# Performance work log

Hardware: AMD Instinct MI355X
Metric: run time of the kernel (lower is better)

Reference implementation:

```python
import jax, jax.numpy as jnp
import numpy as np
import math

C = 768; H = 12; B = 2; TX = 2048; TC = 2048

def setup_inputs() -> dict:
    key = jax.random.key(0)
    ks = jax.random.split(key, 20)
    w = lambda k, s: jax.random.normal(k, s, dtype=jnp.float32) * 0.02
    inp = {
        "x": jax.random.normal(ks[0], (B, TX, C), dtype=jnp.float32),
        "context": jax.random.normal(ks[1], (B, TC, C), dtype=jnp.float32),
        "ln1_g": jnp.ones((C,), jnp.float32), "ln1_b": jnp.zeros((C,), jnp.float32),
        "ln2_g": jnp.ones((C,), jnp.float32), "ln2_b": jnp.zeros((C,), jnp.float32),
        "ln3_g": jnp.ones((C,), jnp.float32), "ln3_b": jnp.zeros((C,), jnp.float32),
        "sa_wq": w(ks[2], (C, C)), "sa_bq": jnp.zeros((C,), jnp.float32),
        "sa_wk": w(ks[3], (C, C)), "sa_bk": jnp.zeros((C,), jnp.float32),
        "sa_wv": w(ks[4], (C, C)), "sa_bv": jnp.zeros((C,), jnp.float32),
        "sa_wo": w(ks[5], (C, C)), "sa_bo": jnp.zeros((C,), jnp.float32),
        "xa_wq": w(ks[6], (C, C)), "xa_bq": jnp.zeros((C,), jnp.float32),
        "xa_wk": w(ks[7], (C, C)), "xa_bk": jnp.zeros((C,), jnp.float32),
        "xa_wv": w(ks[8], (C, C)), "xa_bv": jnp.zeros((C,), jnp.float32),
        "xa_wo": w(ks[9], (C, C)), "xa_bo": jnp.zeros((C,), jnp.float32),
        "mlp_w1": w(ks[10], (C, 4 * C)), "mlp_b1": jnp.zeros((4 * C,), jnp.float32),
        "mlp_w2": w(ks[11], (4 * C, C)), "mlp_b2": jnp.zeros((C,), jnp.float32),
        "n_head": H,
    }
    return inp

def _layernorm(x, g, b, eps=1e-5):
    mu = jnp.mean(x, axis=-1, keepdims=True)
    var = jnp.mean(jnp.square(x - mu), axis=-1, keepdims=True)
    return (x - mu) * jax.lax.rsqrt(var + eps) * g + b

def _attn(xq, xkv, wq, bq, wk, bk, wv, bv, wo, bo, n_head):
    Bq, Tq, Cm = xq.shape
    Tk = xkv.shape[1]
    dh = Cm // n_head
    q = (xq @ wq + bq).reshape(Bq, Tq, n_head, dh)
    k = (xkv @ wk + bk).reshape(Bq, Tk, n_head, dh)
    v = (xkv @ wv + bv).reshape(Bq, Tk, n_head, dh)
    att = jnp.einsum('bqhd,bkhd->bhqk', q, k) * (1.0 / math.sqrt(dh))
    att = jax.nn.softmax(att, axis=-1)
    y = jnp.einsum('bhqk,bkhd->bqhd', att, v).reshape(Bq, Tq, Cm)
    return y @ wo + bo

def reference(x, context, ln1_g, ln1_b, ln2_g, ln2_b, ln3_g, ln3_b,
              sa_wq, sa_bq, sa_wk, sa_bk, sa_wv, sa_bv, sa_wo, sa_bo,
              xa_wq, xa_bq, xa_wk, xa_bk, xa_wv, xa_bv, xa_wo, xa_bo,
              mlp_w1, mlp_b1, mlp_w2, mlp_b2, n_head):
    # pre-LN residual self-attention
    x = x + _attn(_layernorm(x, ln1_g, ln1_b), _layernorm(x, ln1_g, ln1_b),
                  sa_wq, sa_bq, sa_wk, sa_bk, sa_wv, sa_bv, sa_wo, sa_bo, n_head)
    # pre-LN residual cross-attention (context not normalized, matching source)
    x = x + _attn(_layernorm(x, ln2_g, ln2_b), context,
                  xa_wq, xa_bq, xa_wk, xa_bk, xa_wv, xa_bv, xa_wo, xa_bo, n_head)
    # pre-LN residual MLP with exact (erf) GELU, as torch.nn.GELU default
    h = _layernorm(x, ln3_g, ln3_b)
    x = x + (jax.nn.gelu(h @ mlp_w1 + mlp_b1, approximate=False) @ mlp_w2 + mlp_b2)
    return (x, context)
```

## Files before the change

kernel.cpp:

```cpp
#include <hip/hip_runtime.h>
#include <hip/hip_bf16.h>
#include <math.h>

#define CDIM 768
#define HDIM 3072
#define NROWS 4096
#define TSEQ 2048
#define NHEAD 12

typedef unsigned short u16;
typedef unsigned int   u32;
typedef __attribute__((ext_vector_type(8))) short short8;
typedef __attribute__((ext_vector_type(4))) float f32x4;

#define QSCALE 0.18033688011112042f

static __device__ __forceinline__ u16 f2bf(float f) {
    u32 x = __float_as_uint(f);
    x += 0x7fffu + ((x >> 16) & 1u);
    return (u16)(x >> 16);
}
static __device__ __forceinline__ u32 cvt_pk_bf16(float lo, float hi) {
    u32 r;
    asm("v_cvt_pk_bf16_f32 %0, %1, %2" : "=v"(r) : "v"(lo), "v"(hi));
    return r;
}

#define GLL16(g, l)                                                            \
    __builtin_amdgcn_global_load_lds(                                          \
        (const __attribute__((address_space(1))) void*)(g),                    \
        (__attribute__((address_space(3))) void*)(l), 16, 0, 0)

__launch_bounds__(256)
__global__ void wtrans(const float* __restrict__ w, u16* __restrict__ wt,
                       int K, int N) {
    __shared__ float t[32][33];
    const int n0 = blockIdx.x * 32, k0 = blockIdx.y * 32;
    const int tx = threadIdx.x & 31, ty = threadIdx.x >> 5;
#pragma unroll
    for (int i = ty; i < 32; i += 8)
        t[i][tx] = w[(size_t)(k0 + i) * N + n0 + tx];
    __syncthreads();
#pragma unroll
    for (int i = ty; i < 32; i += 8)
        wt[(size_t)(n0 + i) * K + k0 + tx] = f2bf(t[tx][i]);
}

__launch_bounds__(256)
__global__ void cvt_copy(const float* __restrict__ in, u16* __restrict__ out,
                         int n4) {
    int i = blockIdx.x * 256 + threadIdx.x;
    if (i >= n4) return;
    float4 v = ((const float4*)in)[i];
    ushort4 o;
    o.x = f2bf(v.x); o.y = f2bf(v.y); o.z = f2bf(v.z); o.w = f2bf(v.w);
    ((ushort4*)out)[i] = o;
}

__launch_bounds__(256)
__global__ void ln_kernel(const float* __restrict__ x, const float* __restrict__ g,
                          const float* __restrict__ bta, u16* __restrict__ out) {
    const int row = blockIdx.x, tid = threadIdx.x;
    const float* xr = x + (size_t)row * CDIM;
    float v0 = xr[tid], v1 = xr[tid + 256], v2 = xr[tid + 512];
    __shared__ float red[8];
    float s = v0 + v1 + v2;
#pragma unroll
    for (int m = 1; m < 64; m <<= 1) s += __shfl_xor(s, m);
    if ((tid & 63) == 0) red[tid >> 6] = s;
    __syncthreads();
    const float mu = (red[0] + red[1] + red[2] + red[3]) * (1.f / CDIM);
    const float d0 = v0 - mu, d1 = v1 - mu, d2 = v2 - mu;
    float q = d0 * d0 + d1 * d1 + d2 * d2;
#pragma unroll
    for (int m = 1; m < 64; m <<= 1) q += __shfl_xor(q, m);
    if ((tid & 63) == 0) red[4 + (tid >> 6)] = q;
    __syncthreads();
    const float var = (red[4] + red[5] + red[6] + red[7]) * (1.f / CDIM);
    const float rstd = rsqrtf(var + 1e-5f);
    u16* orow = out + (size_t)row * CDIM;
    orow[tid]       = f2bf(d0 * rstd * g[tid]       + bta[tid]);
    orow[tid + 256] = f2bf(d1 * rstd * g[tid + 256] + bta[tid + 256]);
    orow[tid + 512] = f2bf(d2 * rstd * g[tid + 512] + bta[tid + 512]);
}

struct GemmArgs {
    const u16* A[3];
    const u16* BT[3];
    const float* bias[3];
    const float* res[3];
    void* out[3];
    float alpha[3];
    int M, N, K;
};

template <int EPI, int BM>
__launch_bounds__(256)
__global__ void gemm_bt(GemmArgs ga) {
    constexpr int MF = BM / 32;
    __shared__ u16 Abuf[BM * 32];
    __shared__ u16 Bbuf[128 * 32];
    const int z = blockIdx.z;
    const u16* __restrict__ A  = ga.A[z];
    const u16* __restrict__ BT = ga.BT[z];
    const float* __restrict__ bias = ga.bias[z];
    const float* __restrict__ res  = ga.res[z];
    void* outv = ga.out[z];
    const float alpha = ga.alpha[z];
    const int N = ga.N, K = ga.K;

    const int tid = threadIdx.x;
    const int lane = tid & 63, w = tid >> 6;
    const int m0 = blockIdx.x * BM, n0 = blockIdx.y * 128;
    const int wr = (w >> 1) * (BM / 2), wc = (w & 1) * 64;
    const int lr = lane & 15, lc = lane >> 4;

    const int srowA = w * (BM / 4) + (lane >> 2);
    const int srowB = w * 32 + (lane >> 2);
    const int scol = (lane & 3) * 8;
    const u16* Ag = A + (size_t)(m0 + srowA) * K + scol;
    const u16* Bg = BT + (size_t)(n0 + srowB) * K + scol;
    char* Ab = (char*)Abuf + w * (BM * 16);
    char* Bb = (char*)Bbuf + w * 2048;

    f32x4 acc[MF][4];
#pragma unroll
    for (int m = 0; m < MF; ++m)
#pragma unroll
        for (int n = 0; n < 4; ++n) acc[m][n] = (f32x4){0.f, 0.f, 0.f, 0.f};

    const int nk = K >> 5;
    for (int kt = 0; kt < nk; ++kt) {
        const int ko = kt * 32;
        GLL16(Ag + ko, Ab);
        if constexpr (BM == 128) GLL16(Ag + 16 * K + ko, Ab + 1024);
        GLL16(Bg + ko,          Bb);
        GLL16(Bg + 16 * K + ko, Bb + 1024);
        __syncthreads();
        short8 af[MF], bfv[4];
#pragma unroll
        for (int m = 0; m < MF; ++m)
            af[m] = *(const short8*)((const char*)Abuf +
                                     (size_t)(wr + m * 16 + lr) * 64 + lc * 16);
#pragma unroll
        for (int n = 0; n < 4; ++n)
            bfv[n] = *(const short8*)((const char*)Bbuf +
                                      (size_t)(wc + n * 16 + lr) * 64 + lc * 16);
#pragma unroll
        for (int m = 0; m < MF; ++m)
#pragma unroll
            for (int n = 0; n < 4; ++n)
                acc[m][n] = __builtin_amdgcn_mfma_f32_16x16x32_bf16(
                    af[m], bfv[n], acc[m][n], 0, 0, 0);
        __syncthreads();
    }

#pragma unroll
    for (int n = 0; n < 4; ++n) {
        const int gc = n0 + wc + n * 16 + lr;
        const float bs = bias[gc];
#pragma unroll
        for (int m = 0; m < MF; ++m) {
            const int gr = m0 + wr + m * 16 + lc * 4;
#pragma unroll
            for (int r = 0; r < 4; ++r) {
                float v = (acc[m][n][r] + bs) * alpha;
                const size_t idx = (size_t)(gr + r) * N + gc;
                if constexpr (EPI == 0) {
                    ((u16*)outv)[idx] = f2bf(v);
                } else if constexpr (EPI == 1) {
                    ((float*)outv)[idx] = res[idx] + v;
                } else {
                    float gel = 0.5f * v * (1.0f + erff(v * 0.70710678118654752f));
                    ((u16*)outv)[idx] = f2bf(gel);
                }
            }
        }
    }
}

__launch_bounds__(256)
__global__ void attn_kernel(const u16* __restrict__ Qb, const u16* __restrict__ Kb,
                            const u16* __restrict__ Vb, u16* __restrict__ Ob) {
    __shared__ u16 Klds[64 * 72];
    __shared__ u16 Vt[64 * 72];
    const int tid = threadIdx.x;
    const int lane = tid & 63, w = tid >> 6;
    const int lr = lane & 15, lc = lane >> 4;
    const int b = blockIdx.y / NHEAD, h = blockIdx.y % NHEAD;
    const size_t qrow0 = (size_t)b * TSEQ + blockIdx.x * 64 + w * 16;
    const size_t krow0 = (size_t)b * TSEQ;
    const int hc = h * 64;

    short8 qf0, qf1;
    {
        const u16* qp = Qb + (qrow0 + lr) * CDIM + hc + lc * 8;
        qf0 = *(const short8*)qp;
        qf1 = *(const short8*)(qp + 32);
    }
    f32x4 oacc[4];
#pragma unroll
    for (int r = 0; r < 4; ++r) oacc[r] = (f32x4){0.f, 0.f, 0.f, 0.f};
    float mrow = -3e38f, lrow = 0.f;

    const int stg_r = tid >> 2, stg_s = tid & 3;
    const u16* kg = Kb + (krow0 + stg_r) * CDIM + hc + stg_s * 16;
    const u16* vg = Vb + (krow0 + stg_r) * CDIM + hc + stg_s * 16;
    uint4 ka0 = *(const uint4*)kg, ka1 = *(const uint4*)(kg + 8);
    uint4 va0 = *(const uint4*)vg, va1 = *(const uint4*)(vg + 8);
    const int sig = ((stg_r >> 5) << 5) + (((stg_r >> 2) & 3) << 3) +
                    (((stg_r >> 4) & 1) << 2) + (stg_r & 3);
    char* vdst = (char*)Vt + ((2 * sig) ^ (stg_s << 5)) +
                 (size_t)(stg_s * 16) * 144;

    for (int kt = 0; kt < TSEQ / 64; ++kt) {
        __syncthreads();
        {
            *(uint4*)&Klds[stg_r * 72 + stg_s * 16]     = ka0;
            *(uint4*)&Klds[stg_r * 72 + stg_s * 16 + 8] = ka1;
            u16 tmp[16];
            *(uint4*)(tmp)     = va0;
            *(uint4*)(tmp + 8) = va1;
#pragma unroll
            for (int j = 0; j < 16; ++j)
                *(u16*)(vdst + (size_t)j * 144) = tmp[j];
        }
        if (kt < TSEQ / 64 - 1) {
            kg += 64 * CDIM; vg += 64 * CDIM;
            ka0 = *(const uint4*)kg; ka1 = *(const uint4*)(kg + 8);
            va0 = *(const uint4*)vg; va1 = *(const uint4*)(vg + 8);
        }
        __syncthreads();

        f32x4 sf[4];
#pragma unroll
        for (int fn = 0; fn < 4; ++fn) {
            const u16* kr = &Klds[(lr + fn * 16) * 72 + lc * 8];
            short8 kb0 = *(const short8*)kr;
            short8 kb1 = *(const short8*)(kr + 32);
            f32x4 t = (f32x4){0.f, 0.f, 0.f, 0.f};
            t = __builtin_amdgcn_mfma_f32_16x16x32_bf16(kb0, qf0, t, 0, 0, 0);
            t = __builtin_amdgcn_mfma_f32_16x16x32_bf16(kb1, qf1, t, 0, 0, 0);
            sf[fn] = t;
        }

        float pm;
        {
            float a0 = fmaxf(fmaxf(sf[0][0], sf[0][1]), fmaxf(sf[0][2], sf[0][3]));
            float a1 = fmaxf(fmaxf(sf[1][0], sf[1][1]), fmaxf(sf[1][2], sf[1][3]));
            float a2 = fmaxf(fmaxf(sf[2][0], sf[2][1]), fmaxf(sf[2][2], sf[2][3]));
            float a3 = fmaxf(fmaxf(sf[3][0], sf[3][1]), fmaxf(sf[3][2], sf[3][3]));
            pm = fmaxf(fmaxf(a0, a1), fmaxf(a2, a3));
            pm = fmaxf(pm, __shfl_xor(pm, 16));
            pm = fmaxf(pm, __shfl_xor(pm, 32));
        }
        const float mn = fmaxf(mrow, pm);
        const float corr = exp2f(mrow - mn);
        mrow = mn;
        float rs;
        {
#pragma unroll
            for (int fn = 0; fn < 4; ++fn)
#pragma unroll
                for (int r = 0; r < 4; ++r) sf[fn][r] = exp2f(sf[fn][r] - mn);
            float s0 = (sf[0][0] + sf[0][1]) + (sf[0][2] + sf[0][3]);
            float s1 = (sf[1][0] + sf[1][1]) + (sf[1][2] + sf[1][3]);
            float s2 = (sf[2][0] + sf[2][1]) + (sf[2][2] + sf[2][3]);
            float s3 = (sf[3][0] + sf[3][1]) + (sf[3][2] + sf[3][3]);
            rs = (s0 + s1) + (s2 + s3);
            rs += __shfl_xor(rs, 16);
            rs += __shfl_xor(rs, 32);
        }
        lrow = lrow * corr + rs;
#pragma unroll
        for (int fd = 0; fd < 4; ++fd)
#pragma unroll
            for (int r = 0; r < 4; ++r) oacc[fd][r] *= corr;

        int4 pw0, pw1;
        pw0.x = cvt_pk_bf16(sf[0][0], sf[0][1]);
        pw0.y = cvt_pk_bf16(sf[0][2], sf[0][3]);
        pw0.z = cvt_pk_bf16(sf[1][0], sf[1][1]);
        pw0.w = cvt_pk_bf16(sf[1][2], sf[1][3]);
        pw1.x = cvt_pk_bf16(sf[2][0], sf[2][1]);
        pw1.y = cvt_pk_bf16(sf[2][2], sf[2][3]);
        pw1.z = cvt_pk_bf16(sf[3][0], sf[3][1]);
        pw1.w = cvt_pk_bf16(sf[3][2], sf[3][3]);
        short8 pb0 = *(short8*)&pw0;
        short8 pb1 = *(short8*)&pw1;

#pragma unroll
        for (int fd = 0; fd < 4; ++fd) {
            const char* vtb = (const char*)Vt + (size_t)(lr + fd * 16) * 144;
            short8 vb0 = *(const short8*)(vtb + ((lc * 16) ^ (fd * 32)));
            short8 vb1 = *(const short8*)(vtb + ((lc * 16 + 64) ^ (fd * 32)));
            oacc[fd] = __builtin_amdgcn_mfma_f32_16x16x32_bf16(vb0, pb0, oacc[fd], 0, 0, 0);
            oacc[fd] = __builtin_amdgcn_mfma_f32_16x16x32_bf16(vb1, pb1, oacc[fd], 0, 0, 0);
        }
    }

    const float rl = 1.f / lrow;
    u16* obase = Ob + (qrow0 + lr) * CDIM + hc + lc * 4;
#pragma unroll
    for (int fd = 0; fd < 4; ++fd) {
        ushort4 o;
        o.x = f2bf(oacc[fd][0] * rl);
        o.y = f2bf(oacc[fd][1] * rl);
        o.z = f2bf(oacc[fd][2] * rl);
        o.w = f2bf(oacc[fd][3] * rl);
        *(ushort4*)(obase + fd * 16) = o;
    }
}

extern "C" void kernel_launch(void* const* d_in, const int* in_sizes, int n_in,
                              void* d_out, int out_size, void* d_ws, size_t ws_size,
                              hipStream_t stream) {
    const float* x     = (const float*)d_in[0];
    const float* ctx   = (const float*)d_in[1];
    const float* ln1g  = (const float*)d_in[2];
    const float* ln1b  = (const float*)d_in[3];
    const float* ln2g  = (const float*)d_in[4];
    const float* ln2b  = (const float*)d_in[5];
    const float* ln3g  = (const float*)d_in[6];
    const float* ln3b  = (const float*)d_in[7];
    const float* sa_wq = (const float*)d_in[8];
    const float* sa_bq = (const float*)d_in[9];
    const float* sa_wk = (const float*)d_in[10];
    const float* sa_bk = (const float*)d_in[11];
    const float* sa_wv = (const float*)d_in[12];
    const float* sa_bv = (const float*)d_in[13];
    const float* sa_wo = (const float*)d_in[14];
    const float* sa_bo = (const float*)d_in[15];
    const float* xa_wq = (const float*)d_in[16];
    const float* xa_bq = (const float*)d_in[17];
    const float* xa_wk = (const float*)d_in[18];
    const float* xa_bk = (const float*)d_in[19];
    const float* xa_wv = (const float*)d_in[20];
    const float* xa_bv = (const float*)d_in[21];
    const float* xa_wo = (const float*)d_in[22];
    const float* xa_bo = (const float*)d_in[23];
    const float* m_w1  = (const float*)d_in[24];
    const float* m_b1  = (const float*)d_in[25];
    const float* m_w2  = (const float*)d_in[26];
    const float* m_b2  = (const float*)d_in[27];

    float* out_x   = (float*)d_out;
    float* out_ctx = out_x + (size_t)NROWS * CDIM;

    const size_t SZ_ACT  = (size_t)NROWS * CDIM * 2;
    const size_t SZ_WBIG = (size_t)HDIM * CDIM * 2;
    const size_t SZ_R    = (size_t)NROWS * CDIM * 4;
    const size_t NEEDED  = 5 * SZ_ACT + SZ_R + SZ_WBIG;
    if (ws_size < NEEDED) return;

    char* ws = (char*)d_ws;
    u16* qb    = (u16*)(ws);
    u16* kb    = (u16*)(ws + 1 * SZ_ACT);
    u16* vb    = (u16*)(ws + 2 * SZ_ACT);
    u16* ctxb  = (u16*)(ws + 3 * SZ_ACT);
    u16* hb    = qb;
    u16* lnbuf = (u16*)(ws + 4 * SZ_ACT);
    u16* attB  = lnbuf;
    float* R   = (float*)(ws + 5 * SZ_ACT);
    u16* Wq    = (u16*)(ws + 5 * SZ_ACT + SZ_R);
    u16* Wk    = Wq + (size_t)CDIM * CDIM;
    u16* Wv    = Wk + (size_t)CDIM * CDIM;

    const dim3 tb(256);
    GemmArgs ga;

    hipMemcpyAsync(out_ctx, ctx, (size_t)NROWS * CDIM * 4,
                   hipMemcpyDeviceToDevice, stream);
    cvt_copy<<<dim3(3072), tb, 0, stream>>>(ctx, ctxb, NROWS * CDIM / 4);

    ln_kernel<<<dim3(NROWS), tb, 0, stream>>>(x, ln1g, ln1b, lnbuf);
    wtrans<<<dim3(24, 24), tb, 0, stream>>>(sa_wq, Wq, 768, 768);
    wtrans<<<dim3(24, 24), tb, 0, stream>>>(sa_wk, Wk, 768, 768);
    wtrans<<<dim3(24, 24), tb, 0, stream>>>(sa_wv, Wv, 768, 768);
    ga = GemmArgs{};
    ga.A[0] = lnbuf; ga.BT[0] = Wq; ga.bias[0] = sa_bq; ga.out[0] = qb; ga.alpha[0] = QSCALE;
    ga.A[1] = lnbuf; ga.BT[1] = Wk; ga.bias[1] = sa_bk; ga.out[1] = kb; ga.alpha[1] = 1.f;
    ga.A[2] = lnbuf; ga.BT[2] = Wv; ga.bias[2] = sa_bv; ga.out[2] = vb; ga.alpha[2] = 1.f;
    ga.M = 4096; ga.N = 768; ga.K = 768;
    gemm_bt<0, 128><<<dim3(32, 6, 3), tb, 0, stream>>>(ga);
    attn_kernel<<<dim3(32, 24), tb, 0, stream>>>(qb, kb, vb, attB);
    wtrans<<<dim3(24, 24), tb, 0, stream>>>(sa_wo, Wq, 768, 768);
    ga = GemmArgs{};
    ga.A[0] = attB; ga.BT[0] = Wq; ga.bias[0] = sa_bo; ga.res[0] = x; ga.out[0] = R; ga.alpha[0] = 1.f;
    ga.M = 4096; ga.N = 768; ga.K = 768;
    gemm_bt<1, 64><<<dim3(64, 6, 1), tb, 0, stream>>>(ga);

    ln_kernel<<<dim3(NROWS), tb, 0, stream>>>(R, ln2g, ln2b, lnbuf);
    wtrans<<<dim3(24, 24), tb, 0, stream>>>(xa_wq, Wq, 768, 768);
    wtrans<<<dim3(24, 24), tb, 0, stream>>>(xa_wk, Wk, 768, 768);
    wtrans<<<dim3(24, 24), tb, 0, stream>>>(xa_wv, Wv, 768, 768);
    ga = GemmArgs{};
    ga.A[0] = lnbuf; ga.BT[0] = Wq; ga.bias[0] = xa_bq; ga.out[0] = qb; ga.alpha[0] = QSCALE;
    ga.A[1] = ctxb;  ga.BT[1] = Wk; ga.bias[1] = xa_bk; ga.out[1] = kb; ga.alpha[1] = 1.f;
    ga.A[2] = ctxb;  ga.BT[2] = Wv; ga.bias[2] = xa_bv; ga.out[2] = vb; ga.alpha[2] = 1.f;
    ga.M = 4096; ga.N = 768; ga.K = 768;
    gemm_bt<0, 128><<<dim3(32, 6, 3), tb, 0, stream>>>(ga);
    attn_kernel<<<dim3(32, 24), tb, 0, stream>>>(qb, kb, vb, attB);
    wtrans<<<dim3(24, 24), tb, 0, stream>>>(xa_wo, Wq, 768, 768);
    ga = GemmArgs{};
    ga.A[0] = attB; ga.BT[0] = Wq; ga.bias[0] = xa_bo; ga.res[0] = R; ga.out[0] = R; ga.alpha[0] = 1.f;
    ga.M = 4096; ga.N = 768; ga.K = 768;
    gemm_bt<1, 64><<<dim3(64, 6, 1), tb, 0, stream>>>(ga);

    ln_kernel<<<dim3(NROWS), tb, 0, stream>>>(R, ln3g, ln3b, lnbuf);
    wtrans<<<dim3(96, 24), tb, 0, stream>>>(m_w1, Wq, 768, 3072);
    ga = GemmArgs{};
    ga.A[0] = lnbuf; ga.BT[0] = Wq; ga.bias[0] = m_b1; ga.out[0] = hb; ga.alpha[0] = 1.f;
    ga.M = 4096; ga.N = 3072; ga.K = 768;
    gemm_bt<2, 128><<<dim3(32, 24, 1), tb, 0, stream>>>(ga);
    wtrans<<<dim3(24, 96), tb, 0, stream>>>(m_w2, Wq, 3072, 768);
    ga = GemmArgs{};
    ga.A[0] = hb; ga.BT[0] = Wq; ga.bias[0] = m_b2; ga.res[0] = R; ga.out[0] = out_x; ga.alpha[0] = 1.f;
    ga.M = 4096; ga.N = 768; ga.K = 3072;
    gemm_bt<1, 64><<<dim3(64, 6, 1), tb, 0, stream>>>(ga);

    (void)in_sizes; (void)n_in; (void)out_size;
}
```

Before: 394.8 us.

## Split attention over KV halves with a separate softmax merge kernel

Attention now runs as a split-KV (flash-decoding style) pass. Each block handles half of the key/value sequence and writes unnormalized fp32 partial outputs plus per-row max and sum into the output buffer and the weight scratch. A merge kernel then rescales the two halves and writes the bf16 result. This doubles the block count from 768 to 1536 to improve occupancy across CUs. The cost is extra fp32 partial traffic and one extra launch per attention, and the context copy into the output is moved later so the partial buffers can reuse that space.

```diff
diff --git a/kernel.cpp b/kernel.cpp
--- a/kernel.cpp
+++ b/kernel.cpp
@@ -7,6 +7,8 @@
 #define NROWS 4096
 #define TSEQ 2048
 #define NHEAD 12
+#define KVSPLIT 2
+#define KVLEN (TSEQ / KVSPLIT)
 
 typedef unsigned short u16;
 typedef unsigned int   u32;
@@ -180,16 +182,18 @@
 }
 
 __launch_bounds__(256)
-__global__ void attn_kernel(const u16* __restrict__ Qb, const u16* __restrict__ Kb,
-                            const u16* __restrict__ Vb, u16* __restrict__ Ob) {
+__global__ void attn_split(const u16* __restrict__ Qb, const u16* __restrict__ Kb,
+                           const u16* __restrict__ Vb, float* __restrict__ Opart,
+                           float2* __restrict__ ml) {
     __shared__ u16 Klds[64 * 72];
     __shared__ u16 Vt[64 * 72];
     const int tid = threadIdx.x;
     const int lane = tid & 63, w = tid >> 6;
     const int lr = lane & 15, lc = lane >> 4;
     const int b = blockIdx.y / NHEAD, h = blockIdx.y % NHEAD;
+    const int z = blockIdx.z;
     const size_t qrow0 = (size_t)b * TSEQ + blockIdx.x * 64 + w * 16;
-    const size_t krow0 = (size_t)b * TSEQ;
+    const size_t krow0 = (size_t)b * TSEQ + (size_t)z * KVLEN;
     const int hc = h * 64;
 
     short8 qf0, qf1;
@@ -213,7 +217,7 @@
     char* vdst = (char*)Vt + ((2 * sig) ^ (stg_s << 5)) +
                  (size_t)(stg_s * 16) * 144;
 
-    for (int kt = 0; kt < TSEQ / 64; ++kt) {
+    for (int kt = 0; kt < KVLEN / 64; ++kt) {
         __syncthreads();
         {
             *(uint4*)&Klds[stg_r * 72 + stg_s * 16]     = ka0;
@@ -225,7 +229,7 @@
             for (int j = 0; j < 16; ++j)
                 *(u16*)(vdst + (size_t)j * 144) = tmp[j];
         }
-        if (kt < TSEQ / 64 - 1) {
+        if (kt < KVLEN / 64 - 1) {
             kg += 64 * CDIM; vg += 64 * CDIM;
             ka0 = *(const uint4*)kg; ka1 = *(const uint4*)(kg + 8);
             va0 = *(const uint4*)vg; va1 = *(const uint4*)(vg + 8);
@@ -299,17 +303,36 @@
         }
     }
 
-    const float rl = 1.f / lrow;
-    u16* obase = Ob + (qrow0 + lr) * CDIM + hc + lc * 4;
+    float* obase = Opart + (size_t)z * NROWS * CDIM + (qrow0 + lr) * CDIM + hc + lc * 4;
 #pragma unroll
     for (int fd = 0; fd < 4; ++fd) {
-        ushort4 o;
-        o.x = f2bf(oacc[fd][0] * rl);
-        o.y = f2bf(oacc[fd][1] * rl);
-        o.z = f2bf(oacc[fd][2] * rl);
-        o.w = f2bf(oacc[fd][3] * rl);
-        *(ushort4*)(obase + fd * 16) = o;
+        float4 o = {oacc[fd][0], oacc[fd][1], oacc[fd][2], oacc[fd][3]};
+        *(float4*)(obase + fd * 16) = o;
     }
+    if (lc == 0)
+        ml[((size_t)z * NROWS + qrow0 + lr) * NHEAD + h] = (float2){mrow, lrow};
+}
+
+__launch_bounds__(256)
+__global__ void attn_merge(const float* __restrict__ P0, const float* __restrict__ P1,
+                           const float2* __restrict__ ml, u16* __restrict__ out) {
+    const int i4 = blockIdx.x * 256 + threadIdx.x;
+    const size_t base = (size_t)i4 * 4;
+    const int row = (int)(base / CDIM);
+    const int head = (int)(base - (size_t)row * CDIM) >> 6;
+    const float2 a = ml[(size_t)row * NHEAD + head];
+    const float2 c = ml[((size_t)NROWS + row) * NHEAD + head];
+    const float M = fmaxf(a.x, c.x);
+    const float e0 = exp2f(a.x - M), e1 = exp2f(c.x - M);
+    const float rden = 1.f / (a.y * e0 + c.y * e1);
+    const float4 p0 = *(const float4*)(P0 + base);
+    const float4 p1 = *(const float4*)(P1 + base);
+    ushort4 o;
+    o.x = f2bf((p0.x * e0 + p1.x * e1) * rden);
+    o.y = f2bf((p0.y * e0 + p1.y * e1) * rden);
+    o.z = f2bf((p0.z * e0 + p1.z * e1) * rden);
+    o.w = f2bf((p0.w * e0 + p1.w * e1) * rden);
+    *(ushort4*)(out + base) = o;
 }
 
 extern "C" void kernel_launch(void* const* d_in, const int* in_sizes, int n_in,
@@ -346,6 +369,7 @@
 
     float* out_x   = (float*)d_out;
     float* out_ctx = out_x + (size_t)NROWS * CDIM;
+    float* Opart   = (float*)d_out;
 
     const size_t SZ_ACT  = (size_t)NROWS * CDIM * 2;
     const size_t SZ_WBIG = (size_t)HDIM * CDIM * 2;
@@ -365,12 +389,11 @@
     u16* Wq    = (u16*)(ws + 5 * SZ_ACT + SZ_R);
     u16* Wk    = Wq + (size_t)CDIM * CDIM;
     u16* Wv    = Wk + (size_t)CDIM * CDIM;
+    float2* ml = (float2*)Wq;
 
     const dim3 tb(256);
     GemmArgs ga;
 
-    hipMemcpyAsync(out_ctx, ctx, (size_t)NROWS * CDIM * 4,
-                   hipMemcpyDeviceToDevice, stream);
     cvt_copy<<<dim3(3072), tb, 0, stream>>>(ctx, ctxb, NROWS * CDIM / 4);
 
     ln_kernel<<<dim3(NROWS), tb, 0, stream>>>(x, ln1g, ln1b, lnbuf);
@@ -383,7 +406,9 @@
     ga.A[2] = lnbuf; ga.BT[2] = Wv; ga.bias[2] = sa_bv; ga.out[2] = vb; ga.alpha[2] = 1.f;
     ga.M = 4096; ga.N = 768; ga.K = 768;
     gemm_bt<0, 128><<<dim3(32, 6, 3), tb, 0, stream>>>(ga);
-    attn_kernel<<<dim3(32, 24), tb, 0, stream>>>(qb, kb, vb, attB);
+    attn_split<<<dim3(32, 24, KVSPLIT), tb, 0, stream>>>(qb, kb, vb, Opart, ml);
+    attn_merge<<<dim3(NROWS * CDIM / 1024), tb, 0, stream>>>(
+        Opart, Opart + (size_t)NROWS * CDIM, ml, attB);
     wtrans<<<dim3(24, 24), tb, 0, stream>>>(sa_wo, Wq, 768, 768);
     ga = GemmArgs{};
     ga.A[0] = attB; ga.BT[0] = Wq; ga.bias[0] = sa_bo; ga.res[0] = x; ga.out[0] = R; ga.alpha[0] = 1.f;
@@ -400,7 +425,11 @@
     ga.A[2] = ctxb;  ga.BT[2] = Wv; ga.bias[2] = xa_bv; ga.out[2] = vb; ga.alpha[2] = 1.f;
     ga.M = 4096; ga.N = 768; ga.K = 768;
     gemm_bt<0, 128><<<dim3(32, 6, 3), tb, 0, stream>>>(ga);
-    attn_kernel<<<dim3(32, 24), tb, 0, stream>>>(qb, kb, vb, attB);
+    attn_split<<<dim3(32, 24, KVSPLIT), tb, 0, stream>>>(qb, kb, vb, Opart, ml);
+    attn_merge<<<dim3(NROWS * CDIM / 1024), tb, 0, stream>>>(
+        Opart, Opart + (size_t)NROWS * CDIM, ml, attB);
+    hipMemcpyAsync(out_ctx, ctx, (size_t)NROWS * CDIM * 4,
+                   hipMemcpyDeviceToDevice, stream);
     wtrans<<<dim3(24, 24), tb, 0, stream>>>(xa_wo, Wq, 768, 768);
     ga = GemmArgs{};
     ga.A[0] = attB; ga.BT[0] = Wq; ga.bias[0] = xa_bo; ga.res[0] = R; ga.out[0] = R; ga.alpha[0] = 1.f;
```

Result: no change. 392.4 us (-0.6%).
